# Optimization experiments

Measured on AMD Instinct MI355X. Metric: run time of the kernel, lower is better.

## Reference

```python
import jax, jax.numpy as jnp
import numpy as np

N_EMBD = 256
N_HEAD = 8
BATCH = 4
SEQ = 2048
NEG_BIAS = -1000000000.0


def setup_inputs() -> dict:
    key = jax.random.key(0)
    ks = jax.random.split(key, 5)
    scale = 1.0 / np.sqrt(N_EMBD)
    x = jax.random.normal(ks[0], (BATCH, SEQ, N_EMBD), dtype=jnp.float32)
    # torch Linear weight layout: (out_features, in_features)
    Wq = jax.random.normal(ks[1], (N_EMBD * N_HEAD, N_EMBD), dtype=jnp.float32) * scale
    Wk = jax.random.normal(ks[2], (N_EMBD * N_HEAD, N_EMBD), dtype=jnp.float32) * scale
    Wv = jax.random.normal(ks[3], (N_EMBD * N_HEAD, N_EMBD), dtype=jnp.float32) * scale
    Wo = jax.random.normal(ks[4], (N_EMBD, N_EMBD * N_HEAD), dtype=jnp.float32) * scale / np.sqrt(N_HEAD)
    return {"x": x, "Wq": Wq, "Wk": Wk, "Wv": Wv, "Wo": Wo}


def reference(x, Wq, Wk, Wv, Wo):
    B, L, E = x.shape
    H, D = N_HEAD, N_EMBD  # d_head == n_embd in this module
    # projections: x @ W.T, then split heads -> (B, H, L, D)
    def proj(W):
        y = jnp.einsum('ble,fe->blf', x, W)  # (B, L, H*D)
        return y.reshape(B, L, H, D).transpose(0, 2, 1, 3)
    q, k, v = proj(Wq), proj(Wk), proj(Wv)
    scores = jnp.einsum('bhld,bhmd->bhlm', q, k) * (E ** -0.5)
    # first (non-causal) softmax over full rows
    attn = jax.nn.softmax(scores, axis=-1)
    # causal mask replaces disallowed probs with large negative bias, then softmax again
    causal = jnp.tril(jnp.ones((L, L), dtype=bool))
    attn = jnp.where(causal[None, None], attn, jnp.asarray(NEG_BIAS, attn.dtype))
    attn = jax.nn.softmax(attn, axis=-1)
    out = jnp.einsum('bhlm,bhmd->bhld', attn, v)  # (B, H, L, D)
    out = out.transpose(0, 2, 1, 3).reshape(B, L, H * D)
    return jnp.einsum('blf,ef->ble', out, Wo)  # (B, L, E)
```

## Files before the change

### kernel.cpp

```cpp
#include <hip/hip_runtime.h>
#include <stdint.h>

typedef unsigned short ushort_t;
typedef __attribute__((ext_vector_type(8))) short bf16x8;
typedef __attribute__((ext_vector_type(4))) float f32x4;
typedef __attribute__((ext_vector_type(4))) unsigned short us4;

#define DEV __device__ __forceinline__

DEV ushort_t f2bf(float f) {
    unsigned int u = __float_as_uint(f);
    u += 0x7fffu + ((u >> 16) & 1u);
    return (ushort_t)(u >> 16);
}

DEV void async16(const ushort_t* g, ushort_t* l) {
    __builtin_amdgcn_global_load_lds(
        (const __attribute__((address_space(1))) void*)g,
        (__attribute__((address_space(3))) void*)l,
        16, 0, 0);
}

__global__ void convert_kernel(const float* __restrict__ x, const float* __restrict__ wq,
                               const float* __restrict__ wk, const float* __restrict__ wv,
                               const float* __restrict__ wo,
                               ushort_t* __restrict__ xb, ushort_t* __restrict__ wqb,
                               ushort_t* __restrict__ wkb, ushort_t* __restrict__ wvb,
                               ushort_t* __restrict__ wob)
{
    const int i = blockIdx.x * 256 + threadIdx.x;
    const float* src; ushort_t* dst; int off;
    if (i < 524288)      { src = x;  dst = xb;  off = i; }
    else if (i < 655360) { src = wq; dst = wqb; off = i - 524288; }
    else if (i < 786432) { src = wk; dst = wkb; off = i - 655360; }
    else if (i < 917504) { src = wv; dst = wvb; off = i - 786432; }
    else                 { src = wo; dst = wob; off = i - 917504; }
    const float4 v = ((const float4*)src)[off];
    us4 o;
    o[0] = f2bf(v.x); o[1] = f2bf(v.y); o[2] = f2bf(v.z); o[3] = f2bf(v.w);
    ((us4*)dst)[off] = o;
}

template <int MODE>
__global__ __launch_bounds__(256, 2) void gemm_bt_kernel(
    const ushort_t* __restrict__ A, const ushort_t* __restrict__ Bm,
    void* __restrict__ Cout, int M, int N, int K)
{
    __shared__ ushort_t At[128 * 64];
    __shared__ ushort_t Bt[128 * 64];

    const int tid  = threadIdx.x;
    const int wave = tid >> 6;
    const int lane = tid & 63;
    const int quad = lane >> 4;
    const int l15  = lane & 15;
    const int mhalf = wave >> 1;
    const int nhalf = wave & 1;
    const int m0 = blockIdx.x * 128;
    const int n0 = blockIdx.y * 128;

    f32x4 acc[4][4];
#pragma unroll
    for (int mf = 0; mf < 4; ++mf)
#pragma unroll
        for (int nf = 0; nf < 4; ++nf)
#pragma unroll
            for (int r = 0; r < 4; ++r) acc[mf][nf][r] = 0.f;

    const int crow = (lane & 7) ^ (lane >> 3);

    for (int k0 = 0; k0 < K; k0 += 64) {
        __syncthreads();
#pragma unroll
        for (int t = 0; t < 4; ++t) {
            const int row = wave * 32 + t * 8 + (lane >> 3);
            async16(A + (size_t)(m0 + row) * K + k0 + crow * 8,
                    At + (wave * 32 + t * 8) * 64 + lane * 8);
            async16(Bm + (size_t)(n0 + row) * K + k0 + crow * 8,
                    Bt + (wave * 32 + t * 8) * 64 + lane * 8);
        }
        __syncthreads();
#pragma unroll
        for (int ks = 0; ks < 2; ++ks) {
            bf16x8 af[4], bf[4];
#pragma unroll
            for (int mf = 0; mf < 4; ++mf) {
                const int ml = mhalf * 64 + mf * 16 + l15;
                const int c = (ks * 4 + quad) ^ (ml & 7);
                af[mf] = *(const bf16x8*)(At + ml * 64 + c * 8);
            }
#pragma unroll
            for (int nf = 0; nf < 4; ++nf) {
                const int nl = nhalf * 64 + nf * 16 + l15;
                const int c = (ks * 4 + quad) ^ (nl & 7);
                bf[nf] = *(const bf16x8*)(Bt + nl * 64 + c * 8);
            }
#pragma unroll
            for (int mf = 0; mf < 4; ++mf)
#pragma unroll
                for (int nf = 0; nf < 4; ++nf)
                    acc[mf][nf] = __builtin_amdgcn_mfma_f32_16x16x32_bf16(
                        af[mf], bf[nf], acc[mf][nf], 0, 0, 0);
        }
    }

    if (MODE == 1) {
#pragma unroll
        for (int mf = 0; mf < 4; ++mf)
#pragma unroll
            for (int nf = 0; nf < 4; ++nf) {
                const int row = m0 + mhalf * 64 + mf * 16 + quad * 4;
                const int col = n0 + nhalf * 64 + nf * 16 + l15;
                const int b_ = row >> 11, l_ = row & 2047;
                const int h_ = col >> 8, d_ = col & 255;
                us4 pk;
#pragma unroll
                for (int r = 0; r < 4; ++r) pk[r] = f2bf(acc[mf][nf][r]);
                *(us4*)((ushort_t*)Cout +
                        (((size_t)(b_ * 8 + h_) * 256 + d_) * 2048 + l_)) = pk;
            }
    } else {
#pragma unroll
        for (int mf = 0; mf < 4; ++mf)
#pragma unroll
            for (int nf = 0; nf < 4; ++nf)
#pragma unroll
                for (int r = 0; r < 4; ++r) {
                    const int row = m0 + mhalf * 64 + mf * 16 + quad * 4 + r;
                    const int col = n0 + nhalf * 64 + nf * 16 + l15;
                    if (MODE == 0)
                        ((ushort_t*)Cout)[(size_t)row * N + col] = f2bf(acc[mf][nf][r]);
                    else
                        ((float*)Cout)[(size_t)row * N + col] = acc[mf][nf][r];
                }
    }
}

__global__ __launch_bounds__(256, 4) void pass1_kernel(
    const ushort_t* __restrict__ q_ws, const ushort_t* __restrict__ k_ws,
    float* __restrict__ rz_ws)
{
    __shared__ ushort_t Kt[64 * 256];
    __shared__ float zred[2][64];

    const float SCALE = 0.0625f;
    const int tid  = threadIdx.x;
    const int wave = tid >> 6;
    const int lane = tid & 63;
    const int quad = lane >> 4;
    const int l15  = lane & 15;
    const int ihalf = wave >> 1;
    const int jhalf = wave & 1;

    const int g  = blockIdx.x;
    const int bh = ((g >> 8) << 3) | (g & 7);
    const int it = (g >> 3) & 31;
    const int b = bh >> 3, h = bh & 7;
    const int i0 = it * 64;

    const size_t qkbase = (size_t)b * 2048 * 2048 + (size_t)h * 256;

    bf16x8 qf[2][8];
#pragma unroll
    for (int ng = 0; ng < 2; ++ng) {
        const int i_l = ihalf * 32 + ng * 16 + l15;
        const ushort_t* qr = q_ws + qkbase + (size_t)(i0 + i_l) * 2048;
#pragma unroll
        for (int ks = 0; ks < 8; ++ks)
            qf[ng][ks] = *(const bf16x8*)(qr + ks * 32 + quad * 8);
    }

    float z[2] = {0.f, 0.f};

    for (int jt = 0; jt < 32; ++jt) {
        const int j0 = jt * 64;
        __syncthreads();
        {
            const ushort_t* kb = k_ws + qkbase + (size_t)j0 * 2048;
#pragma unroll
            for (int t = 0; t < 8; ++t) {
                const int row = wave * 16 + t * 2 + (lane >> 5);
                const int c = (lane & 31) ^ (row & 7);
                async16(kb + (size_t)row * 2048 + c * 8,
                        Kt + (wave * 16 + t * 2) * 256 + lane * 8);
            }
        }
        __syncthreads();

        f32x4 sacc[2][2];
#pragma unroll
        for (int a = 0; a < 2; ++a)
#pragma unroll
            for (int c = 0; c < 2; ++c)
#pragma unroll
                for (int r = 0; r < 4; ++r) sacc[a][c][r] = 0.f;

#pragma unroll
        for (int ks = 0; ks < 8; ++ks) {
            bf16x8 af[2];
#pragma unroll
            for (int mg = 0; mg < 2; ++mg) {
                const int j_l = jhalf * 32 + mg * 16 + l15;
                const int c = (ks * 4 + quad) ^ (j_l & 7);
                af[mg] = *(const bf16x8*)(Kt + j_l * 256 + c * 8);
            }
#pragma unroll
            for (int mg = 0; mg < 2; ++mg)
#pragma unroll
                for (int ng = 0; ng < 2; ++ng)
                    sacc[mg][ng] = __builtin_amdgcn_mfma_f32_16x16x32_bf16(
                        af[mg], qf[ng][ks], sacc[mg][ng], 0, 0, 0);
        }

#pragma unroll
        for (int ng = 0; ng < 2; ++ng)
#pragma unroll
            for (int mg = 0; mg < 2; ++mg)
#pragma unroll
                for (int r = 0; r < 4; ++r)
                    z[ng] += __expf(sacc[mg][ng][r] * SCALE);
    }

#pragma unroll
    for (int ng = 0; ng < 2; ++ng) {
        z[ng] += __shfl_xor(z[ng], 16);
        z[ng] += __shfl_xor(z[ng], 32);
    }
    __syncthreads();
    if (quad == 0) {
#pragma unroll
        for (int ng = 0; ng < 2; ++ng) {
            const int i_l = ihalf * 32 + ng * 16 + l15;
            zred[jhalf][i_l] = z[ng];
        }
    }
    __syncthreads();
    if (tid < 64)
        rz_ws[(size_t)bh * 2048 + i0 + tid] = 1.0f / (zred[0][tid] + zred[1][tid]);
}

__global__ __launch_bounds__(256, 2) void pass2_kernel(
    const ushort_t* __restrict__ q_ws, const ushort_t* __restrict__ k_ws,
    const ushort_t* __restrict__ vt_ws, const float* __restrict__ rz_ws,
    ushort_t* __restrict__ attn_out)
{
    __shared__ ushort_t smem[36864];
    ushort_t* Kt = smem;
    ushort_t* Vt = smem + 16384;
    ushort_t* Wt = smem + 32768;

    const float SCALE = 0.0625f;
    const int tid  = threadIdx.x;
    const int wave = tid >> 6;
    const int lane = tid & 63;
    const int quad = lane >> 4;
    const int l15  = lane & 15;
    const int ihalf = wave >> 1;
    const int jhalf = wave & 1;

    const int g  = blockIdx.x;
    const int bh = ((g >> 8) << 3) | (g & 7);
    const int it = 31 - ((g >> 3) & 31);
    const int b = bh >> 3, h = bh & 7;
    const int i0 = it * 64;

    const size_t qkbase = (size_t)b * 2048 * 2048 + (size_t)h * 256;

    bf16x8 qf[2][8];
#pragma unroll
    for (int ng = 0; ng < 2; ++ng) {
        const int i_l = ihalf * 32 + ng * 16 + l15;
        const ushort_t* qr = q_ws + qkbase + (size_t)(i0 + i_l) * 2048;
#pragma unroll
        for (int ks = 0; ks < 8; ++ks)
            qf[ng][ks] = *(const bf16x8*)(qr + ks * 32 + quad * 8);
    }

    float rzrow[2];
#pragma unroll
    for (int ng = 0; ng < 2; ++ng) {
        const int i_l = ihalf * 32 + ng * 16 + l15;
        rzrow[ng] = rz_ws[(size_t)bh * 2048 + i0 + i_l];
    }

    f32x4 oacc[2][8];
#pragma unroll
    for (int mg = 0; mg < 2; ++mg)
#pragma unroll
        for (int nf = 0; nf < 8; ++nf)
#pragma unroll
            for (int r = 0; r < 4; ++r) oacc[mg][nf][r] = 0.f;
    float den[2] = {0.f, 0.f};

    for (int jt = 0; jt <= it; ++jt) {
        const int j0 = jt * 64;
        const bool diag = (jt == it);
        __syncthreads();
        {
            const ushort_t* kb = k_ws + qkbase + (size_t)j0 * 2048;
#pragma unroll
            for (int t = 0; t < 8; ++t) {
                const int row = wave * 16 + t * 2 + (lane >> 5);
                const int c = (lane & 31) ^ (row & 7);
                async16(kb + (size_t)row * 2048 + c * 8,
                        Kt + (wave * 16 + t * 2) * 256 + lane * 8);
            }
            const ushort_t* vb = vt_ws + (size_t)bh * 256 * 2048 + j0;
#pragma unroll
            for (int t = 0; t < 8; ++t) {
                const int row = wave * 64 + t * 8 + (lane >> 3);
                const int c = (lane & 7) ^ (row & 7);
                async16(vb + (size_t)row * 2048 + c * 8,
                        Vt + (wave * 64 + t * 8) * 64 + lane * 8);
            }
        }
        __syncthreads();

        f32x4 sacc[2][2];
#pragma unroll
        for (int a = 0; a < 2; ++a)
#pragma unroll
            for (int c = 0; c < 2; ++c)
#pragma unroll
                for (int r = 0; r < 4; ++r) sacc[a][c][r] = 0.f;

#pragma unroll
        for (int ks = 0; ks < 8; ++ks) {
            bf16x8 af[2];
#pragma unroll
            for (int mg = 0; mg < 2; ++mg) {
                const int j_l = jhalf * 32 + mg * 16 + l15;
                const int c = (ks * 4 + quad) ^ (j_l & 7);
                af[mg] = *(const bf16x8*)(Kt + j_l * 256 + c * 8);
            }
#pragma unroll
            for (int mg = 0; mg < 2; ++mg)
#pragma unroll
                for (int ng = 0; ng < 2; ++ng)
                    sacc[mg][ng] = __builtin_amdgcn_mfma_f32_16x16x32_bf16(
                        af[mg], qf[ng][ks], sacc[mg][ng], 0, 0, 0);
        }

#pragma unroll
        for (int mg = 0; mg < 2; ++mg) {
#pragma unroll
            for (int ng = 0; ng < 2; ++ng) {
                const int i_l = ihalf * 32 + ng * 16 + l15;
                const int jb = jhalf * 32 + mg * 16 + quad * 4;
                us4 wp;
#pragma unroll
                for (int r = 0; r < 4; ++r) {
                    const float p = __expf(sacc[mg][ng][r] * SCALE) * rzrow[ng];
                    float w = __expf(p);
                    if (diag && (jb + r > i_l)) w = 0.f;
                    den[ng] += w;
                    wp[r] = f2bf(w);
                }
                const int c = (jb >> 3) ^ (i_l & 7);
                *(us4*)(Wt + i_l * 64 + c * 8 + (jb & 7)) = wp;
            }
        }
        __syncthreads();

#pragma unroll
        for (int ks = 0; ks < 2; ++ks) {
            bf16x8 aw[2];
#pragma unroll
            for (int mg = 0; mg < 2; ++mg) {
                const int i_l = ihalf * 32 + mg * 16 + l15;
                const int c = (ks * 4 + quad) ^ (i_l & 7);
                aw[mg] = *(const bf16x8*)(Wt + i_l * 64 + c * 8);
            }
#pragma unroll
            for (int nf = 0; nf < 8; ++nf) {
                const int d = jhalf * 128 + nf * 16 + l15;
                const int c = (ks * 4 + quad) ^ (d & 7);
                const bf16x8 bv = *(const bf16x8*)(Vt + d * 64 + c * 8);
                oacc[0][nf] = __builtin_amdgcn_mfma_f32_16x16x32_bf16(aw[0], bv, oacc[0][nf], 0, 0, 0);
                oacc[1][nf] = __builtin_amdgcn_mfma_f32_16x16x32_bf16(aw[1], bv, oacc[1][nf], 0, 0, 0);
            }
        }
    }

    __syncthreads();
    {
        float* dbuf = (float*)Kt;
#pragma unroll
        for (int ng = 0; ng < 2; ++ng) {
            const int i_l = ihalf * 32 + ng * 16 + l15;
            dbuf[(jhalf * 4 + quad) * 64 + i_l] = den[ng];
        }
    }
    __syncthreads();
    if (tid < 64) {
        const float* dbuf = (const float*)Kt;
        float s = 0.f;
#pragma unroll
        for (int p = 0; p < 8; ++p) s += dbuf[p * 64 + tid];
        ((float*)Kt)[512 + tid] = 1.0f / s;
    }
    __syncthreads();
    {
        const float* rden = (const float*)Kt + 512;
#pragma unroll
        for (int mg = 0; mg < 2; ++mg) {
#pragma unroll
            for (int r = 0; r < 4; ++r) {
                const int i_l = ihalf * 32 + mg * 16 + quad * 4 + r;
                const float rd = rden[i_l];
                ushort_t* orow = attn_out + qkbase + (size_t)(i0 + i_l) * 2048;
#pragma unroll
                for (int nf = 0; nf < 8; ++nf) {
                    const int d = jhalf * 128 + nf * 16 + l15;
                    orow[d] = f2bf(oacc[mg][nf][r] * rd);
                }
            }
        }
    }
}

extern "C" void kernel_launch(void* const* d_in, const int* in_sizes, int n_in,
                              void* d_out, int out_size, void* d_ws, size_t ws_size,
                              hipStream_t stream) {
    const float* x  = (const float*)d_in[0];
    const float* Wq = (const float*)d_in[1];
    const float* Wk = (const float*)d_in[2];
    const float* Wv = (const float*)d_in[3];
    const float* Wo = (const float*)d_in[4];

    char* ws = (char*)d_ws;
    ushort_t* xb    = (ushort_t*)(ws);
    ushort_t* wqb   = (ushort_t*)(ws + 4194304);
    ushort_t* wkb   = (ushort_t*)(ws + 5242880);
    ushort_t* wvb   = (ushort_t*)(ws + 6291456);
    ushort_t* wob   = (ushort_t*)(ws + 7340032);
    ushort_t* q_ws  = (ushort_t*)(ws + 8388608);
    ushort_t* k_ws  = (ushort_t*)(ws + 41943040);
    ushort_t* vt_ws = (ushort_t*)(ws + 75497472);
    ushort_t* ao_ws = (ushort_t*)(ws + 109051904);
    float*    rz_ws = (float*)   (ws + 142606336);

    convert_kernel<<<4096, 256, 0, stream>>>(x, Wq, Wk, Wv, Wo, xb, wqb, wkb, wvb, wob);

    dim3 gp(64, 16);
    gemm_bt_kernel<0><<<gp, 256, 0, stream>>>(xb, wqb, q_ws, 8192, 2048, 256);
    gemm_bt_kernel<0><<<gp, 256, 0, stream>>>(xb, wkb, k_ws, 8192, 2048, 256);
    gemm_bt_kernel<1><<<gp, 256, 0, stream>>>(xb, wvb, vt_ws, 8192, 2048, 256);

    pass1_kernel<<<1024, 256, 0, stream>>>(q_ws, k_ws, rz_ws);
    pass2_kernel<<<1024, 256, 0, stream>>>(q_ws, k_ws, vt_ws, rz_ws, ao_ws);

    gemm_bt_kernel<2><<<dim3(64, 2), 256, 0, stream>>>(ao_ws, wob, d_out, 8192, 256, 2048);
}
```

Before: 356.6 us.

## Fuse QKV projections, split-K attention waves, smaller-tile output GEMM

Merges the three Q/K/V projection GEMMs into one launch over a concatenated N=6144, which relies on wqb/wkb/wvb sitting contiguously in the workspace. Restructures pass2 so each wave keeps its own P tile in LDS and computes all 256 output columns over its half of the key tile. This removes a block-wide sync per tile and lets one wave skip the fully masked diagonal quadrant, at the cost of more accumulator registers and a cross-wave reduction at the end. Replaces the output projection with a 64x128-tile kernel to launch more blocks on the K=2048 GEMM.

```diff
diff --git a/kernel.cpp b/kernel.cpp
--- a/kernel.cpp
+++ b/kernel.cpp
@@ -3,6 +3,7 @@
 
 typedef unsigned short ushort_t;
 typedef __attribute__((ext_vector_type(8))) short bf16x8;
+typedef __attribute__((ext_vector_type(4))) short s16x4;
 typedef __attribute__((ext_vector_type(4))) float f32x4;
 typedef __attribute__((ext_vector_type(4))) unsigned short us4;
 
@@ -44,7 +45,8 @@
 template <int MODE>
 __global__ __launch_bounds__(256, 2) void gemm_bt_kernel(
     const ushort_t* __restrict__ A, const ushort_t* __restrict__ Bm,
-    void* __restrict__ Cout, int M, int N, int K)
+    void* __restrict__ C0, void* __restrict__ C1, void* __restrict__ C2,
+    int M, int N, int K)
 {
     __shared__ ushort_t At[128 * 64];
     __shared__ ushort_t Bt[128 * 64];
@@ -104,21 +106,36 @@
         }
     }
 
-    if (MODE == 1) {
-#pragma unroll
-        for (int mf = 0; mf < 4; ++mf)
-#pragma unroll
-            for (int nf = 0; nf < 4; ++nf) {
-                const int row = m0 + mhalf * 64 + mf * 16 + quad * 4;
-                const int col = n0 + nhalf * 64 + nf * 16 + l15;
-                const int b_ = row >> 11, l_ = row & 2047;
-                const int h_ = col >> 8, d_ = col & 255;
-                us4 pk;
-#pragma unroll
-                for (int r = 0; r < 4; ++r) pk[r] = f2bf(acc[mf][nf][r]);
-                *(us4*)((ushort_t*)Cout +
-                        (((size_t)(b_ * 8 + h_) * 256 + d_) * 2048 + l_)) = pk;
-            }
+    if (MODE == 3) {
+        const int sel = n0 >> 11;
+        if (sel == 2) {
+#pragma unroll
+            for (int mf = 0; mf < 4; ++mf)
+#pragma unroll
+                for (int nf = 0; nf < 4; ++nf) {
+                    const int row = m0 + mhalf * 64 + mf * 16 + quad * 4;
+                    const int colv = (n0 - 4096) + nhalf * 64 + nf * 16 + l15;
+                    const int b_ = row >> 11, l_ = row & 2047;
+                    const int h_ = colv >> 8, d_ = colv & 255;
+                    us4 pk;
+#pragma unroll
+                    for (int r = 0; r < 4; ++r) pk[r] = f2bf(acc[mf][nf][r]);
+                    *(us4*)((ushort_t*)C2 +
+                            (((size_t)(b_ * 8 + h_) * 256 + d_) * 2048 + l_)) = pk;
+                }
+        } else {
+            ushort_t* dst = sel ? (ushort_t*)C1 : (ushort_t*)C0;
+#pragma unroll
+            for (int mf = 0; mf < 4; ++mf)
+#pragma unroll
+                for (int nf = 0; nf < 4; ++nf)
+#pragma unroll
+                    for (int r = 0; r < 4; ++r) {
+                        const int row = m0 + mhalf * 64 + mf * 16 + quad * 4 + r;
+                        const int col = (n0 & 2047) + nhalf * 64 + nf * 16 + l15;
+                        dst[(size_t)row * 2048 + col] = f2bf(acc[mf][nf][r]);
+                    }
+        }
     } else {
 #pragma unroll
         for (int mf = 0; mf < 4; ++mf)
@@ -128,12 +145,87 @@
                 for (int r = 0; r < 4; ++r) {
                     const int row = m0 + mhalf * 64 + mf * 16 + quad * 4 + r;
                     const int col = n0 + nhalf * 64 + nf * 16 + l15;
-                    if (MODE == 0)
-                        ((ushort_t*)Cout)[(size_t)row * N + col] = f2bf(acc[mf][nf][r]);
-                    else
-                        ((float*)Cout)[(size_t)row * N + col] = acc[mf][nf][r];
+                    ((float*)C0)[(size_t)row * N + col] = acc[mf][nf][r];
                 }
     }
+}
+
+__global__ __launch_bounds__(256, 4) void gemm_out_kernel(
+    const ushort_t* __restrict__ A, const ushort_t* __restrict__ Bm,
+    float* __restrict__ C)
+{
+    __shared__ ushort_t At[64 * 64];
+    __shared__ ushort_t Bt[128 * 64];
+
+    const int tid  = threadIdx.x;
+    const int wave = tid >> 6;
+    const int lane = tid & 63;
+    const int quad = lane >> 4;
+    const int l15  = lane & 15;
+    const int mhalf = wave >> 1;
+    const int nhalf = wave & 1;
+    const int m0 = blockIdx.x * 64;
+    const int n0 = blockIdx.y * 128;
+
+    f32x4 acc[2][4];
+#pragma unroll
+    for (int mf = 0; mf < 2; ++mf)
+#pragma unroll
+        for (int nf = 0; nf < 4; ++nf)
+#pragma unroll
+            for (int r = 0; r < 4; ++r) acc[mf][nf][r] = 0.f;
+
+    const int crow = (lane & 7) ^ (lane >> 3);
+
+    for (int k0 = 0; k0 < 2048; k0 += 64) {
+        __syncthreads();
+#pragma unroll
+        for (int t = 0; t < 2; ++t) {
+            const int row = wave * 16 + t * 8 + (lane >> 3);
+            async16(A + (size_t)(m0 + row) * 2048 + k0 + crow * 8,
+                    At + (wave * 16 + t * 8) * 64 + lane * 8);
+        }
+#pragma unroll
+        for (int t = 0; t < 4; ++t) {
+            const int row = wave * 32 + t * 8 + (lane >> 3);
+            async16(Bm + (size_t)(n0 + row) * 2048 + k0 + crow * 8,
+                    Bt + (wave * 32 + t * 8) * 64 + lane * 8);
+        }
+        __syncthreads();
+#pragma unroll
+        for (int ks = 0; ks < 2; ++ks) {
+            bf16x8 af[2], bf[4];
+#pragma unroll
+            for (int mf = 0; mf < 2; ++mf) {
+                const int ml = mhalf * 32 + mf * 16 + l15;
+                const int c = (ks * 4 + quad) ^ (ml & 7);
+                af[mf] = *(const bf16x8*)(At + ml * 64 + c * 8);
+            }
+#pragma unroll
+            for (int nf = 0; nf < 4; ++nf) {
+                const int nl = nhalf * 64 + nf * 16 + l15;
+                const int c = (ks * 4 + quad) ^ (nl & 7);
+                bf[nf] = *(const bf16x8*)(Bt + nl * 64 + c * 8);
+            }
+#pragma unroll
+            for (int mf = 0; mf < 2; ++mf)
+#pragma unroll
+                for (int nf = 0; nf < 4; ++nf)
+                    acc[mf][nf] = __builtin_amdgcn_mfma_f32_16x16x32_bf16(
+                        af[mf], bf[nf], acc[mf][nf], 0, 0, 0);
+        }
+    }
+
+#pragma unroll
+    for (int mf = 0; mf < 2; ++mf)
+#pragma unroll
+        for (int nf = 0; nf < 4; ++nf)
+#pragma unroll
+            for (int r = 0; r < 4; ++r) {
+                const int row = m0 + mhalf * 32 + mf * 16 + quad * 4 + r;
+                const int col = n0 + nhalf * 64 + nf * 16 + l15;
+                C[(size_t)row * 256 + col] = acc[mf][nf][r];
+            }
 }
 
 __global__ __launch_bounds__(256, 4) void pass1_kernel(
@@ -283,14 +375,16 @@
         rzrow[ng] = rz_ws[(size_t)bh * 2048 + i0 + i_l];
     }
 
-    f32x4 oacc[2][8];
-#pragma unroll
-    for (int mg = 0; mg < 2; ++mg)
-#pragma unroll
-        for (int nf = 0; nf < 8; ++nf)
-#pragma unroll
-            for (int r = 0; r < 4; ++r) oacc[mg][nf][r] = 0.f;
+    f32x4 oacc[2][16];
+#pragma unroll
+    for (int ng = 0; ng < 2; ++ng)
+#pragma unroll
+        for (int nf = 0; nf < 16; ++nf)
+#pragma unroll
+            for (int r = 0; r < 4; ++r) oacc[ng][nf][r] = 0.f;
     float den[2] = {0.f, 0.f};
+
+    ushort_t* Wp = Wt + wave * 1024;
 
     for (int jt = 0; jt <= it; ++jt) {
         const int j0 = jt * 64;
@@ -315,6 +409,8 @@
             }
         }
         __syncthreads();
+
+        if (diag && ihalf == 0 && jhalf == 1) continue;
 
         f32x4 sacc[2][2];
 #pragma unroll
@@ -356,64 +452,76 @@
                     den[ng] += w;
                     wp[r] = f2bf(w);
                 }
-                const int c = (jb >> 3) ^ (i_l & 7);
-                *(us4*)(Wt + i_l * 64 + c * 8 + (jb & 7)) = wp;
-            }
-        }
-        __syncthreads();
-
-#pragma unroll
-        for (int ks = 0; ks < 2; ++ks) {
-            bf16x8 aw[2];
-#pragma unroll
-            for (int mg = 0; mg < 2; ++mg) {
-                const int i_l = ihalf * 32 + mg * 16 + l15;
-                const int c = (ks * 4 + quad) ^ (i_l & 7);
-                aw[mg] = *(const bf16x8*)(Wt + i_l * 64 + c * 8);
-            }
-#pragma unroll
-            for (int nf = 0; nf < 8; ++nf) {
-                const int d = jhalf * 128 + nf * 16 + l15;
-                const int c = (ks * 4 + quad) ^ (d & 7);
+                const int row = ng * 16 + l15;
+                const int ch = (mg * 4 + quad) ^ (row & 7);
+                *(us4*)(Wp + row * 32 + ch * 4) = wp;
+            }
+        }
+
+#pragma unroll
+        for (int ng = 0; ng < 2; ++ng) {
+            const int row = ng * 16 + l15;
+            const int sw = row & 7;
+            const s16x4 lo = *(const s16x4*)(Wp + row * 32 + ((quad * 2) ^ sw) * 4);
+            const s16x4 hi = *(const s16x4*)(Wp + row * 32 + ((quad * 2 + 1) ^ sw) * 4);
+            union { s16x4 h[2]; bf16x8 v; } u;
+            u.h[0] = lo; u.h[1] = hi;
+            const bf16x8 aw = u.v;
+#pragma unroll
+            for (int nf = 0; nf < 16; ++nf) {
+                const int d = nf * 16 + l15;
+                const int c = (jhalf * 4 + quad) ^ (d & 7);
                 const bf16x8 bv = *(const bf16x8*)(Vt + d * 64 + c * 8);
-                oacc[0][nf] = __builtin_amdgcn_mfma_f32_16x16x32_bf16(aw[0], bv, oacc[0][nf], 0, 0, 0);
-                oacc[1][nf] = __builtin_amdgcn_mfma_f32_16x16x32_bf16(aw[1], bv, oacc[1][nf], 0, 0, 0);
-            }
-        }
-    }
-
+                oacc[ng][nf] = __builtin_amdgcn_mfma_f32_16x16x32_bf16(
+                    aw, bv, oacc[ng][nf], 0, 0, 0);
+            }
+        }
+    }
+
+#pragma unroll
+    for (int ng = 0; ng < 2; ++ng) {
+        den[ng] += __shfl_xor(den[ng], 16);
+        den[ng] += __shfl_xor(den[ng], 32);
+    }
     __syncthreads();
-    {
-        float* dbuf = (float*)Kt;
+    float* mergeb = (float*)smem;
+    float* dbuf   = (float*)(smem + 32768);
+    if (quad == 0) {
+#pragma unroll
+        for (int ng = 0; ng < 2; ++ng)
+            dbuf[(jhalf * 2 + ihalf) * 32 + ng * 16 + l15] = den[ng];
+    }
+    if (jhalf == 1) {
+        float* mb = mergeb + ihalf * 8192;
+#pragma unroll
+        for (int ng = 0; ng < 2; ++ng)
+#pragma unroll
+            for (int nf = 0; nf < 16; ++nf)
+                *(f32x4*)(mb + (ng * 16 + nf) * 256 + lane * 4) = oacc[ng][nf];
+    }
+    __syncthreads();
+    if (jhalf == 0) {
+        const float* mb = mergeb + ihalf * 8192;
+#pragma unroll
+        for (int ng = 0; ng < 2; ++ng)
+#pragma unroll
+            for (int nf = 0; nf < 16; ++nf) {
+                const f32x4 o = *(const f32x4*)(mb + (ng * 16 + nf) * 256 + lane * 4);
+#pragma unroll
+                for (int r = 0; r < 4; ++r) oacc[ng][nf][r] += o[r];
+            }
 #pragma unroll
         for (int ng = 0; ng < 2; ++ng) {
-            const int i_l = ihalf * 32 + ng * 16 + l15;
-            dbuf[(jhalf * 4 + quad) * 64 + i_l] = den[ng];
-        }
-    }
-    __syncthreads();
-    if (tid < 64) {
-        const float* dbuf = (const float*)Kt;
-        float s = 0.f;
-#pragma unroll
-        for (int p = 0; p < 8; ++p) s += dbuf[p * 64 + tid];
-        ((float*)Kt)[512 + tid] = 1.0f / s;
-    }
-    __syncthreads();
-    {
-        const float* rden = (const float*)Kt + 512;
-#pragma unroll
-        for (int mg = 0; mg < 2; ++mg) {
 #pragma unroll
             for (int r = 0; r < 4; ++r) {
-                const int i_l = ihalf * 32 + mg * 16 + quad * 4 + r;
-                const float rd = rden[i_l];
-                ushort_t* orow = attn_out + qkbase + (size_t)(i0 + i_l) * 2048;
-#pragma unroll
-                for (int nf = 0; nf < 8; ++nf) {
-                    const int d = jhalf * 128 + nf * 16 + l15;
-                    orow[d] = f2bf(oacc[mg][nf][r] * rd);
-                }
+                const int il32 = ng * 16 + quad * 4 + r;
+                const float dt = dbuf[ihalf * 32 + il32] + dbuf[(2 + ihalf) * 32 + il32];
+                const float rd = 1.0f / dt;
+                const int i_t = ihalf * 32 + il32;
+                ushort_t* orow = attn_out + qkbase + (size_t)(i0 + i_t) * 2048;
+#pragma unroll
+                for (int nf = 0; nf < 16; ++nf)
+                    orow[nf * 16 + l15] = f2bf(oacc[ng][nf][r] * rd);
             }
         }
     }
@@ -442,13 +550,11 @@
 
     convert_kernel<<<4096, 256, 0, stream>>>(x, Wq, Wk, Wv, Wo, xb, wqb, wkb, wvb, wob);
 
-    dim3 gp(64, 16);
-    gemm_bt_kernel<0><<<gp, 256, 0, stream>>>(xb, wqb, q_ws, 8192, 2048, 256);
-    gemm_bt_kernel<0><<<gp, 256, 0, stream>>>(xb, wkb, k_ws, 8192, 2048, 256);
-    gemm_bt_kernel<1><<<gp, 256, 0, stream>>>(xb, wvb, vt_ws, 8192, 2048, 256);
+    gemm_bt_kernel<3><<<dim3(64, 48), 256, 0, stream>>>(
+        xb, wqb, q_ws, k_ws, vt_ws, 8192, 6144, 256);
 
     pass1_kernel<<<1024, 256, 0, stream>>>(q_ws, k_ws, rz_ws);
     pass2_kernel<<<1024, 256, 0, stream>>>(q_ws, k_ws, vt_ws, rz_ws, ao_ws);
 
-    gemm_bt_kernel<2><<<dim3(64, 2), 256, 0, stream>>>(ao_ws, wob, d_out, 8192, 256, 2048);
-}
+    gemm_out_kernel<<<dim3(128, 2), 256, 0, stream>>>(ao_ws, wob, (float*)d_out);
+}
```

After: 856.3 us. 140% more time.
